# Optimization experiments

Measured on AMD Instinct MI355X. Metric: run time of the kernel, lower is better.

## Reference

```python
import jax, jax.numpy as jnp
import numpy as np

CHANNEL = 256
MEM_SIZE = 684
POS_NUM = 128
NEG_NUM = 512
TEMP = 1.0
CLASS_NUM = 60
BANK_ROWS = MEM_SIZE * CLASS_NUM  # 41040
BATCH = 512


def setup_inputs() -> dict:
    key = jax.random.key(0)
    k1, k2, k3, k4 = jax.random.split(key, 4)
    f = jax.random.normal(k1, (BATCH, CHANNEL), dtype=jnp.float32)
    f_normed = f / jnp.linalg.norm(f, axis=-1, keepdims=True)
    label = jax.random.randint(k2, (BATCH,), 0, CLASS_NUM, dtype=jnp.int32)
    bank = jax.random.normal(k3, (BANK_ROWS, CHANNEL), dtype=jnp.float32)
    bank = bank / jnp.linalg.norm(bank, axis=-1, keepdims=True)
    bank_flag = jnp.ones((BANK_ROWS,), dtype=jnp.float32)  # warmed-up bank
    rand_neg = jax.random.uniform(k4, (BATCH, BANK_ROWS), dtype=jnp.float32)
    # exact torch roundrobin enqueue logic (sequential over the batch)
    rr = np.zeros(CLASS_NUM, dtype=np.int64)
    idxs = []
    for i in np.asarray(label).tolist():
        rr[i] = rr[i] + 1 if rr[i] < CLASS_NUM - 1 else 0
        idxs.append(int(rr[i]) + i * MEM_SIZE)
    enqueue_idx = jnp.asarray(idxs, dtype=jnp.int32)
    return {"f_normed": f_normed, "label": label, "enqueue_idx": enqueue_idx,
            "bank": bank, "bank_flag": bank_flag, "rand_neg": rand_neg}


def reference(f_normed, label, enqueue_idx, bank, bank_flag, rand_neg):
    N = f_normed.shape[0]
    # enqueue (detached write, as in torch: Bank[indies] = f_normed.detach())
    bank = bank.at[enqueue_idx].set(jax.lax.stop_gradient(f_normed))
    flag = bank_flag.at[enqueue_idx].set(1.0)
    # all_pairs: [N, M]
    all_pairs = jnp.einsum('nc,mc->nm', f_normed, bank)
    bank_label = jnp.tile(jnp.arange(CLASS_NUM), MEM_SIZE)  # arange(C).repeat(mem)
    eq = label[:, None] == bank_label[None, :]
    valid = flag > 0
    pos_mask = eq & valid
    neg_mask = (~eq) & valid
    # hard positives: smallest POS_NUM positive similarities per row
    pos_hard = jnp.sort(jnp.where(pos_mask, all_pairs, jnp.inf), axis=-1)[:, :POS_NUM]
    # hard negatives: largest NEG_NUM negative similarities per row
    neg_hard, _ = jax.lax.top_k(jnp.where(neg_mask, all_pairs, -jnp.inf), NEG_NUM)
    # random negatives: uniform sample without replacement via noise argsort
    r = jnp.where(neg_mask, rand_neg, jnp.inf)
    rand_idx = jnp.argsort(r, axis=-1)[:, :NEG_NUM]
    neg_rand = jnp.take_along_axis(all_pairs, rand_idx, axis=-1)
    # combined logits: [N, 2*POS_NUM, 1+NEG_NUM]
    pos = pos_hard[:, :, None]
    h2h = jnp.concatenate([pos, jnp.broadcast_to(neg_hard[:, None, :], (N, POS_NUM, NEG_NUM))], axis=-1)
    h2r = jnp.concatenate([pos, jnp.broadcast_to(neg_rand[:, None, :], (N, POS_NUM, NEG_NUM))], axis=-1)
    combined = jnp.concatenate([h2h, h2r], axis=1).reshape(-1, 1 + NEG_NUM)
    # cross entropy with target class 0 for every row
    loss = -jnp.mean(jax.nn.log_softmax(combined / TEMP, axis=-1)[:, 0])
    return loss
```

## Files before the change

kernel.cpp:

```cpp
#include <hip/hip_runtime.h>

#define CH    256
#define MEM   684
#define POSN  128
#define NEGN  512
#define CLS   60
#define ROWS  41040
#define BATCHN 512

typedef unsigned int u32;
typedef unsigned short u16;
typedef unsigned long long u64;

typedef __attribute__((ext_vector_type(8))) short bf16x8;
typedef __attribute__((ext_vector_type(4))) float f32x4;

__device__ __forceinline__ float b2f(u16 u) { return __uint_as_float(((u32)u) << 16); }
__device__ __forceinline__ u16 f2b(float x) {
  u32 u = __float_as_uint(x);
  u32 r = ((u >> 16) & 1u) + 0x7FFFu;
  return (u16)((u + r) >> 16);
}
__device__ __forceinline__ u32 umin2(u32 a, u32 b) { return a < b ? a : b; }

#if defined(__has_builtin)
#if __has_builtin(__builtin_amdgcn_global_load_lds)
#define HAVE_GLL 1
#endif
#endif

__device__ __forceinline__ void stage16(const u16* g, u16* l) {
#ifdef HAVE_GLL
  __builtin_amdgcn_global_load_lds((const __attribute__((address_space(1))) void*)g,
                                   (__attribute__((address_space(3))) void*)l, 16, 0, 0);
#else
  *(uint4*)l = *(const uint4*)g;
#endif
}

__global__ __launch_bounds__(256) void k_convert(const float* __restrict__ bank,
                                                 u16* __restrict__ bankB) {
  size_t i = (size_t)(blockIdx.x * 256 + threadIdx.x) * 8;
  float4 a = *(const float4*)(bank + i);
  float4 b = *(const float4*)(bank + i + 4);
  uint4 o;
  o.x = (u32)f2b(a.x) | ((u32)f2b(a.y) << 16);
  o.y = (u32)f2b(a.z) | ((u32)f2b(a.w) << 16);
  o.z = (u32)f2b(b.x) | ((u32)f2b(b.y) << 16);
  o.w = (u32)f2b(b.z) | ((u32)f2b(b.w) << 16);
  *(uint4*)(bankB + i) = o;
}

__global__ __launch_bounds__(256) void k_scatter(const float* __restrict__ f,
                                                 const int* __restrict__ enq,
                                                 u16* __restrict__ fB,
                                                 u16* __restrict__ bankB) {
  int n = blockIdx.x, t = threadIdx.x;
  u16 v = f2b(f[n * CH + t]);
  fB[n * CH + t] = v;
  int row = enq[n];
  bankB[(size_t)row * CH + t] = v;
}

__global__ __launch_bounds__(256) void k_gemm(const u16* __restrict__ fB,
                                              const u16* __restrict__ bankB,
                                              u16* __restrict__ Cb) {
  __shared__ __align__(16) u16 As[128 * 32];
  __shared__ __align__(16) u16 Bs[128 * 32];
  const int tid = threadIdx.x;
  const int wave = tid >> 6, lane = tid & 63;

  const u32 id = blockIdx.x;
  const u32 q = 160u, r4 = 4u;
  const u32 xcd = id & 7u, jj = id >> 3;
  const u32 wg = (xcd < r4 ? xcd * (q + 1u) : r4 * (q + 1u) + (xcd - r4) * q) + jj;
  const int bm = (int)(wg & 3u) * 128;
  const int bn = (int)(wg >> 2) * 128;

  const int wm = (wave & 1) * 64, wn = (wave >> 1) * 64;
  const int m_in = lane & 15;
  const int ks = (lane >> 4) * 8;

  f32x4 acc[4][4] = {};

  for (int k0 = 0; k0 < CH; k0 += 32) {
    __syncthreads();
#pragma unroll
    for (int i = 0; i < 2; i++) {
      int u = tid + 256 * i;
      int row = u >> 2;
      int kk = (u & 3) * 8;
      stage16(fB + (size_t)(bm + row) * CH + k0 + kk, As + u * 8);
      int rb = bn + row;
      if (rb >= ROWS) rb = bn;
      stage16(bankB + (size_t)rb * CH + k0 + kk, Bs + u * 8);
    }
    __syncthreads();

    bf16x8 af[4], bf[4];
#pragma unroll
    for (int t4 = 0; t4 < 4; t4++) {
      af[t4] = *(const bf16x8*)(As + (wm + t4 * 16 + m_in) * 32 + ks);
      bf[t4] = *(const bf16x8*)(Bs + (wn + t4 * 16 + m_in) * 32 + ks);
    }
#pragma unroll
    for (int mi = 0; mi < 4; mi++)
#pragma unroll
      for (int ni = 0; ni < 4; ni++)
        acc[mi][ni] = __builtin_amdgcn_mfma_f32_16x16x32_bf16(bf[ni], af[mi], acc[mi][ni], 0, 0, 0);
  }

  const int cc = lane & 15;
  const int rr = (lane >> 4) * 4;
#pragma unroll
  for (int mi = 0; mi < 4; mi++) {
    const int row = bm + wm + mi * 16 + cc;
#pragma unroll
    for (int ni = 0; ni < 4; ni++) {
      const int n0 = bn + wn + ni * 16 + rr;
      if (n0 < ROWS) {
        u64 pk = (u64)f2b(acc[mi][ni][0]) | ((u64)f2b(acc[mi][ni][1]) << 16) |
                 ((u64)f2b(acc[mi][ni][2]) << 32) | ((u64)f2b(acc[mi][ni][3]) << 48);
        *(u64*)(Cb + (size_t)row * ROWS + n0) = pk;
      }
    }
  }
}

__device__ __forceinline__ u32 wscan_incl(u32 v) {
  int lane = (int)(threadIdx.x & 63);
#pragma unroll
  for (int off = 1; off < 64; off <<= 1) {
    u32 t = __shfl_up(v, off, 64);
    if (lane >= off) v += t;
  }
  return v;
}

__device__ __forceinline__ u32 scan1024(u32 v, u32* tmp, int tid) {
  u32 inc = wscan_incl(v);
  int wid = tid >> 6;
  if ((tid & 63) == 63) tmp[wid] = inc;
  __syncthreads();
  if (tid < 64) {
    u32 t = (tid < 16) ? tmp[tid] : 0u;
    u32 ti = wscan_incl(t);
    if (tid < 16) tmp[tid] = ti - t;
  }
  __syncthreads();
  u32 r = inc + tmp[wid];
  __syncthreads();
  return r;
}

__device__ __forceinline__ float redsum1024(float v, float* tmp, int tid) {
#pragma unroll
  for (int off = 32; off > 0; off >>= 1) v += __shfl_xor(v, off, 64);
  int wid = tid >> 6;
  if ((tid & 63) == 0) tmp[wid] = v;
  __syncthreads();
  if (tid == 0) {
    float t = 0.f;
#pragma unroll
    for (int i = 0; i < 16; i++) t += tmp[i];
    tmp[0] = t;
  }
  __syncthreads();
  float r = tmp[0];
  __syncthreads();
  return r;
}

__device__ __forceinline__ int binof(float v, float lo, float scale) {
  int b = (int)((v - lo) * scale);
  return b < 0 ? 0 : (b > 2047 ? 2047 : b);
}

#define VITER 5
#define VTAIL 80
#define VTAILBASE 40960
#define CAPC 3072
#define CAPR 1536

__global__ __launch_bounds__(1024, 8) void k_select(const u16* __restrict__ Cb,
                                                    const float* __restrict__ rnd,
                                                    const int* __restrict__ label,
                                                    float* __restrict__ partial) {
  const int n = blockIdx.x;
  const int tid = threadIdx.x;
  const u16* crow = Cb + (size_t)n * ROWS;
  const float* rrow = rnd + (size_t)n * ROWS;
  const int lab = label[n];

  __shared__ __align__(16) char smem[56448];
  u32* histc = (u32*)(smem);
  u32* histr = (u32*)(smem + 8192);
  float* clist = (float*)(smem + 16384);
  float* rl_rv = (float*)(smem + 28672);
  float* rl_cv = (float*)(smem + 34816);
  u32* rl_mi = (u32*)(smem + 40960);
  u32* stmp = (u32*)(smem + 47104);
  float* fred = (float*)(smem + 47104);
  float* cb_c = (float*)(smem + 51200);
  float* rb_r = (float*)(smem + 53248);
  float* rb_c = (float*)(smem + 54272);
  u32* rb_m = (u32*)(smem + 55296);
  u32* ctl = (u32*)(smem + 56320);
  float* bc_f = (float*)(ctl + 8);

  const int rv0 = (tid * 8) % 60;

  float T1 = 0.09375f;
  float T0 = 0.03125f;
  u32 F = 0, G = 0;
  float sc_c, sc_r;

  for (int attempt = 0;; attempt++) {
    for (int i = tid; i < 2048; i += 1024) { histc[i] = 0; histr[i] = 0; }
    if (tid == 0) { ctl[0] = 0; ctl[1] = 0; }
    __syncthreads();
    sc_c = 2048.0f / (1.0625f - T1);
    sc_r = 2048.0f / T0;
    int rb = rv0;
#pragma unroll 1
    for (int it = 0; it < VITER; it++) {
      int m8 = (it * 1024 + tid) * 8;
      uint4 cr = *(const uint4*)(crow + m8);
      float4 ra = *(const float4*)(rrow + m8);
      float4 rb4 = *(const float4*)(rrow + m8 + 4);
      u32 cw[4] = {cr.x, cr.y, cr.z, cr.w};
      float rs[8] = {ra.x, ra.y, ra.z, ra.w, rb4.x, rb4.y, rb4.z, rb4.w};
      u32 mc = 0, mr = 0;
      int r = rb;
#pragma unroll
      for (int j = 0; j < 8; j++) {
        bool isneg = (r != lab);
        float c = b2f((u16)(cw[j >> 1] >> ((j & 1) * 16)));
        if (isneg && c > T1) mc |= (1u << j);
        if (isneg && rs[j] < T0) mr |= (1u << j);
        r++;
        if (r == 60) r = 0;
      }
      u32 s1 = 0, s2 = 0;
      if (mc) s1 = atomicAdd(&ctl[0], (u32)__popc(mc));
      if (mr) s2 = atomicAdd(&ctl[1], (u32)__popc(mr));
#pragma unroll
      for (int j = 0; j < 8; j++) {
        if (mc & (1u << j)) {
          float c = b2f((u16)(cw[j >> 1] >> ((j & 1) * 16)));
          if (s1 < CAPC) clist[s1] = c;
          atomicAdd(&histc[binof(c, T1, sc_c)], 1u);
          s1++;
        }
        if (mr & (1u << j)) {
          float c = b2f((u16)(cw[j >> 1] >> ((j & 1) * 16)));
          if (s2 < CAPR) { rl_rv[s2] = rs[j]; rl_cv[s2] = c; rl_mi[s2] = (u32)(m8 + j); }
          atomicAdd(&histr[binof(rs[j], 0.0f, sc_r)], 1u);
          s2++;
        }
      }
      rb += 32;
      if (rb >= 60) rb -= 60;
    }
    if (tid < VTAIL) {
      int m = VTAILBASE + tid;
      int r = 40 + tid;
      if (r >= 60) r -= 60;
      bool isneg = (r != lab);
      float c = b2f(crow[m]);
      if (isneg && c > T1) {
        u32 s1 = atomicAdd(&ctl[0], 1u);
        if (s1 < CAPC) clist[s1] = c;
        atomicAdd(&histc[binof(c, T1, sc_c)], 1u);
      }
      float rv = rrow[m];
      if (isneg && rv < T0) {
        u32 s2 = atomicAdd(&ctl[1], 1u);
        if (s2 < CAPR) { rl_rv[s2] = rv; rl_cv[s2] = c; rl_mi[s2] = (u32)m; }
        atomicAdd(&histr[binof(rv, 0.0f, sc_r)], 1u);
      }
    }
    __syncthreads();
    F = ctl[0];
    G = ctl[1];
    __syncthreads();
    if (F >= NEGN && G >= NEGN) break;
    if (F < NEGN) T1 = -1.1f;
    if (G < NEGN) T0 = 1.1f;
  }
  const bool listc_ok = (F <= CAPC);
  const bool listr_ok = (G <= CAPR);

  if (tid == 0) { ctl[2] = 0; ctl[3] = 0; ctl[4] = 0; ctl[5] = 0; ctl[6] = 0; ctl[7] = 0; }
  u32 fsum = histc[tid * 2] + histc[tid * 2 + 1];
  u32 finc = scan1024(fsum, stmp, tid);
  u32 fexc = finc - fsum;
  u32 tcpos = F - NEGN + 1;
  if (fexc < tcpos && tcpos <= finc) {
    u32 run = fexc;
#pragma unroll
    for (int i = 0; i < 2; i++) {
      u32 h = histc[tid * 2 + i];
      if (run + h >= tcpos) { ctl[4] = (u32)(tid * 2 + i); ctl[5] = F - (run + h); break; }
      run += h;
    }
  }
  u32 gsum = histr[tid * 2] + histr[tid * 2 + 1];
  u32 ginc = scan1024(gsum, stmp, tid);
  u32 gexc = ginc - gsum;
  if (gexc < NEGN && NEGN <= ginc) {
    u32 run = gexc;
#pragma unroll
    for (int i = 0; i < 2; i++) {
      u32 h = histr[tid * 2 + i];
      if (run + h >= NEGN) { ctl[6] = (u32)(tid * 2 + i); ctl[7] = run; break; }
      run += h;
    }
  }
  __syncthreads();
  const u32 b_c = ctl[4], cnt_gt = ctl[5];
  const u32 b_r = ctl[6], cnt_lt = ctl[7];
  const u32 need_c = NEGN - cnt_gt;
  const u32 need_r = NEGN - cnt_lt;

  float sH = 0.f, sR = 0.f;
  if (listc_ok) {
    for (u32 i = tid; i < F; i += 1024) {
      float c = clist[i];
      u32 b = (u32)binof(c, T1, sc_c);
      if (b > b_c) sH += expf(c);
      else if (b == b_c) {
        u32 id = atomicAdd(&ctl[2], 1u);
        if (id < 512) cb_c[id] = c;
      }
    }
  }
  if (listr_ok) {
    for (u32 i = tid; i < G; i += 1024) {
      float rv = rl_rv[i];
      u32 b = (u32)binof(rv, 0.0f, sc_r);
      if (b < b_r) sR += expf(rl_cv[i]);
      else if (b == b_r) {
        u32 id = atomicAdd(&ctl[3], 1u);
        if (id < 256) { rb_r[id] = rv; rb_c[id] = rl_cv[i]; rb_m[id] = rl_mi[i]; }
      }
    }
  }
  if (!listc_ok || !listr_ok) {
    for (int m = tid; m < ROWS; m += 1024) {
      int r = m % 60;
      if (r == lab) continue;
      float c = b2f(crow[m]);
      if (!listc_ok && c > T1) {
        u32 b = (u32)binof(c, T1, sc_c);
        if (b > b_c) sH += expf(c);
        else if (b == b_c) {
          u32 id = atomicAdd(&ctl[2], 1u);
          if (id < 512) cb_c[id] = c;
        }
      }
      if (!listr_ok) {
        float rv = rrow[m];
        if (rv < T0) {
          u32 b = (u32)binof(rv, 0.0f, sc_r);
          if (b < b_r) sR += expf(c);
          else if (b == b_r) {
            u32 id = atomicAdd(&ctl[3], 1u);
            if (id < 256) { rb_r[id] = rv; rb_c[id] = c; rb_m[id] = (u32)m; }
          }
        }
      }
    }
  }
  __syncthreads();
  float SHsum = redsum1024(sH, fred, tid);
  float SRsum = redsum1024(sR, fred, tid);

  if (tid == 0) {
    float addH = 0.f;
    u32 Lc = umin2(ctl[2], 512u);
    u32 kc = umin2(need_c, Lc);
    for (u32 k = 0; k < kc; k++) {
      int best = 0;
      float bv = -3.0e38f;
      for (u32 i = 0; i < Lc; i++)
        if (cb_c[i] > bv) { bv = cb_c[i]; best = (int)i; }
      cb_c[best] = -3.0e38f;
      addH += expf(bv);
    }
    u32 Lr = umin2(ctl[3], 256u);
    for (u32 i = 1; i < Lr; i++) {
      float rv = rb_r[i]; u32 mm = rb_m[i]; float cv = rb_c[i];
      int j = (int)i - 1;
      while (j >= 0 && (rb_r[j] > rv || (rb_r[j] == rv && rb_m[j] > mm))) {
        rb_r[j + 1] = rb_r[j]; rb_m[j + 1] = rb_m[j]; rb_c[j + 1] = rb_c[j];
        j--;
      }
      rb_r[j + 1] = rv; rb_m[j + 1] = mm; rb_c[j + 1] = cv;
    }
    float addR = 0.f;
    u32 kr = umin2(need_r, Lr);
    for (u32 i = 0; i < kr; i++) addR += expf(rb_c[i]);
    bc_f[0] = addH;
    bc_f[1] = addR;
  }
  __syncthreads();
  const float S_H = SHsum + bc_f[0];
  const float S_R = SRsum + bc_f[1];
  __syncthreads();

  float pval = 0.f;
  int pbin = 0;
  const bool hasp = tid < MEM;
  const float PLO = -1.03125f;
  const float PSC = 2048.0f / 2.09375f;
  if (hasp) {
    pval = b2f(crow[lab + CLS * tid]);
    pbin = binof(pval, PLO, PSC);
  }
  for (int i = tid; i < 2048; i += 1024) histc[i] = 0;
  if (tid == 0) { ctl[2] = 0; ctl[4] = 0; ctl[5] = 0; }
  __syncthreads();
  if (hasp) atomicAdd(&histc[pbin], 1u);
  __syncthreads();
  u32 hsum = histc[tid * 2] + histc[tid * 2 + 1];
  u32 hinc = scan1024(hsum, stmp, tid);
  u32 hexc = hinc - hsum;
  if (hexc < POSN && POSN <= hinc) {
    u32 run = hexc;
#pragma unroll
    for (int i = 0; i < 2; i++) {
      u32 h = histc[tid * 2 + i];
      if (run + h >= POSN) { ctl[4] = (u32)(tid * 2 + i); ctl[5] = run; break; }
      run += h;
    }
  }
  __syncthreads();
  const u32 b_p = ctl[4], cnt_below = ctl[5];
  const u32 need_p = POSN - cnt_below;
  if (hasp && (u32)pbin == b_p) {
    u32 id = atomicAdd(&ctl[2], 1u);
    if (id < 512) cb_c[id] = pval;
  }
  float term = 0.f;
  if (hasp && (u32)pbin < b_p) {
    float e = expf(pval);
    term = (pval - logf(e + S_H)) + (pval - logf(e + S_R));
  }
  __syncthreads();
  if (tid == 0) {
// ... 13 lines not shown
  }
  __syncthreads();
  float tot = redsum1024(term, fred, tid);
  if (tid == 0) partial[n] = tot + bc_f[0];
}

__global__ __launch_bounds__(256) void k_final(const float* __restrict__ partial,
                                               float* __restrict__ out) {
  __shared__ float fred[256];
  int tid = threadIdx.x;
  float v = partial[tid] + partial[tid + 256];
  fred[tid] = v;
  __syncthreads();
  for (int off = 128; off > 0; off >>= 1) {
    if (tid < off) fred[tid] += fred[tid + off];
    __syncthreads();
  }
  if (tid == 0) out[0] = -fred[0] / (float)(BATCHN * 2 * POSN);
}

extern "C" void kernel_launch(void* const* d_in, const int* in_sizes, int n_in,
                              void* d_out, int out_size, void* d_ws, size_t ws_size,
                              hipStream_t stream) {
  const float* f = (const float*)d_in[0];
  const int* label = (const int*)d_in[1];
  const int* enq = (const int*)d_in[2];
  const float* bank = (const float*)d_in[3];
  const float* rnd = (const float*)d_in[5];
  float* out = (float*)d_out;

  char* ws = (char*)d_ws;
  u16* bankB = (u16*)ws;
  u16* fB = (u16*)(ws + 21012480);
  u16* Cb = (u16*)(ws + 21012480 + 262144);
  float* partial = (float*)(ws + 21012480 + 262144 + 42024960);

  k_convert<<<dim3(5130), dim3(256), 0, stream>>>(bank, bankB);
  k_scatter<<<dim3(BATCHN), dim3(256), 0, stream>>>(f, enq, fB, bankB);
  k_gemm<<<dim3(1284), dim3(256), 0, stream>>>(fB, bankB, Cb);
  k_select<<<dim3(BATCHN), dim3(1024), 0, stream>>>(Cb, rnd, label, partial);
  k_final<<<dim3(1), dim3(256), 0, stream>>>(partial, out);
}
```

Measured before the change: 236.4 us.

## Fuse candidate filtering into GEMM epilogue and compact lists in global memory

The GEMM epilogue now reads the random-noise values, applies the fixed thresholds, and appends hard-negative candidates, random-negative candidates and positive similarities into per-row compacted global lists using atomic counters. The select kernel then builds its histograms from these short lists instead of rescanning the full 41040-element similarity and noise rows, and falls back to the old full scan only when a count is out of range. This trades a second full pass over the similarity and noise matrices for extra reads of the noise matrix, scattered atomics and scattered stores in the GEMM epilogue, plus a memset before launch. List order is now nondeterministic, which may matter only for tie handling.

```diff
diff --git a/kernel.cpp b/kernel.cpp
--- a/kernel.cpp
+++ b/kernel.cpp
@@ -22,6 +22,11 @@
   return (u16)((u + r) >> 16);
 }
 __device__ __forceinline__ u32 umin2(u32 a, u32 b) { return a < b ? a : b; }
+
+#define T1BASE 0.09375f
+#define T0BASE 0.03125f
+#define CAPC 3072
+#define CAPR 1536
 
 #if defined(__has_builtin)
 #if __has_builtin(__builtin_amdgcn_global_load_lds)
@@ -64,7 +69,16 @@
 
 __global__ __launch_bounds__(256) void k_gemm(const u16* __restrict__ fB,
                                               const u16* __restrict__ bankB,
-                                              u16* __restrict__ Cb) {
+                                              const float* __restrict__ rnd,
+                                              const int* __restrict__ label,
+                                              u16* __restrict__ Cb,
+                                              u32* __restrict__ cnt_c,
+                                              u32* __restrict__ cnt_r,
+                                              u16* __restrict__ clist_g,
+                                              float* __restrict__ rrv_g,
+                                              u16* __restrict__ rcv_g,
+                                              u32* __restrict__ rmi_g,
+                                              u16* __restrict__ pos_g) {
   __shared__ __align__(16) u16 As[128 * 32];
   __shared__ __align__(16) u16 Bs[128 * 32];
   const int tid = threadIdx.x;
@@ -115,13 +129,53 @@
 #pragma unroll
   for (int mi = 0; mi < 4; mi++) {
     const int row = bm + wm + mi * 16 + cc;
+    const int labr = label[row];
 #pragma unroll
     for (int ni = 0; ni < 4; ni++) {
       const int n0 = bn + wn + ni * 16 + rr;
       if (n0 < ROWS) {
-        u64 pk = (u64)f2b(acc[mi][ni][0]) | ((u64)f2b(acc[mi][ni][1]) << 16) |
-                 ((u64)f2b(acc[mi][ni][2]) << 32) | ((u64)f2b(acc[mi][ni][3]) << 48);
+        u16 h0 = f2b(acc[mi][ni][0]), h1 = f2b(acc[mi][ni][1]);
+        u16 h2 = f2b(acc[mi][ni][2]), h3 = f2b(acc[mi][ni][3]);
+        u64 pk = (u64)h0 | ((u64)h1 << 16) | ((u64)h2 << 32) | ((u64)h3 << 48);
         *(u64*)(Cb + (size_t)row * ROWS + n0) = pk;
+
+        float4 rv4 = *(const float4*)(rnd + (size_t)row * ROWS + n0);
+        u16 hs[4] = {h0, h1, h2, h3};
+        float rs[4] = {rv4.x, rv4.y, rv4.z, rv4.w};
+        u32 mcc = 0, mrr = 0;
+        int r = n0 % 60;
+#pragma unroll
+        for (int qq = 0; qq < 4; qq++) {
+          bool neg = (r != labr);
+          float cv = b2f(hs[qq]);
+          if (neg && cv > T1BASE) mcc |= (1u << qq);
+          if (neg && rs[qq] < T0BASE) mrr |= (1u << qq);
+          if (r == labr) pos_g[row * MEM + (n0 + qq) / 60] = hs[qq];
+          r++;
+          if (r == 60) r = 0;
+        }
+        if (mcc) {
+          u32 base = atomicAdd(&cnt_c[row], (u32)__popc(mcc));
+#pragma unroll
+          for (int qq = 0; qq < 4; qq++)
+            if (mcc & (1u << qq)) {
+              if (base < CAPC) clist_g[(size_t)row * CAPC + base] = hs[qq];
+              base++;
+            }
+        }
+        if (mrr) {
+          u32 base = atomicAdd(&cnt_r[row], (u32)__popc(mrr));
+#pragma unroll
+          for (int qq = 0; qq < 4; qq++)
+            if (mrr & (1u << qq)) {
+              if (base < CAPR) {
+                rrv_g[(size_t)row * CAPR + base] = rs[qq];
+                rcv_g[(size_t)row * CAPR + base] = hs[qq];
+                rmi_g[(size_t)row * CAPR + base] = (u32)(n0 + qq);
+              }
+              base++;
+            }
+        }
       }
     }
   }
@@ -179,12 +233,17 @@
 #define VITER 5
 #define VTAIL 80
 #define VTAILBASE 40960
-#define CAPC 3072
-#define CAPR 1536
 
 __global__ __launch_bounds__(1024, 8) void k_select(const u16* __restrict__ Cb,
                                                     const float* __restrict__ rnd,
                                                     const int* __restrict__ label,
+                                                    const u32* __restrict__ cnt_c,
+                                                    const u32* __restrict__ cnt_r,
+                                                    const u16* __restrict__ clist_g,
+                                                    const float* __restrict__ rrv_g,
+                                                    const u16* __restrict__ rcv_g,
+                                                    const u32* __restrict__ rmi_g,
+                                                    const u16* __restrict__ pos_g,
                                                     float* __restrict__ partial) {
   const int n = blockIdx.x;
   const int tid = threadIdx.x;
@@ -208,88 +267,101 @@
   u32* ctl = (u32*)(smem + 56320);
   float* bc_f = (float*)(ctl + 8);
 
-  const int rv0 = (tid * 8) % 60;
-
-  float T1 = 0.09375f;
-  float T0 = 0.03125f;
-  u32 F = 0, G = 0;
-  float sc_c, sc_r;
-
-  for (int attempt = 0;; attempt++) {
+  float T1 = T1BASE;
+  float T0 = T0BASE;
+  u32 F = cnt_c[n];
+  u32 G = cnt_r[n];
+  float sc_c = 2048.0f / (1.0625f - T1);
+  float sc_r = 2048.0f / T0;
+  bool listc_ok = true, listr_ok = true;
+  const bool fast = (F >= NEGN && G >= NEGN && F <= CAPC && G <= CAPR);
+
+  if (fast) {
     for (int i = tid; i < 2048; i += 1024) { histc[i] = 0; histr[i] = 0; }
-    if (tid == 0) { ctl[0] = 0; ctl[1] = 0; }
     __syncthreads();
-    sc_c = 2048.0f / (1.0625f - T1);
-    sc_r = 2048.0f / T0;
-    int rb = rv0;
+    for (u32 i = tid; i < F; i += 1024)
+      atomicAdd(&histc[binof(b2f(clist_g[(size_t)n * CAPC + i]), T1, sc_c)], 1u);
+    for (u32 i = tid; i < G; i += 1024)
+      atomicAdd(&histr[binof(rrv_g[(size_t)n * CAPR + i], 0.0f, sc_r)], 1u);
+    __syncthreads();
+  } else {
+    const int rv0 = (tid * 8) % 60;
+    for (int attempt = 0;; attempt++) {
+      for (int i = tid; i < 2048; i += 1024) { histc[i] = 0; histr[i] = 0; }
+      if (tid == 0) { ctl[0] = 0; ctl[1] = 0; }
+      __syncthreads();
+      sc_c = 2048.0f / (1.0625f - T1);
+      sc_r = 2048.0f / T0;
+      int rb = rv0;
 #pragma unroll 1
-    for (int it = 0; it < VITER; it++) {
-      int m8 = (it * 1024 + tid) * 8;
-      uint4 cr = *(const uint4*)(crow + m8);
-      float4 ra = *(const float4*)(rrow + m8);
-      float4 rb4 = *(const float4*)(rrow + m8 + 4);
-      u32 cw[4] = {cr.x, cr.y, cr.z, cr.w};
-      float rs[8] = {ra.x, ra.y, ra.z, ra.w, rb4.x, rb4.y, rb4.z, rb4.w};
-      u32 mc = 0, mr = 0;
-      int r = rb;
-#pragma unroll
-      for (int j = 0; j < 8; j++) {
+      for (int it = 0; it < VITER; it++) {
+        int m8 = (it * 1024 + tid) * 8;
+        uint4 cr = *(const uint4*)(crow + m8);
+        float4 ra = *(const float4*)(rrow + m8);
+        float4 rb4 = *(const float4*)(rrow + m8 + 4);
+        u32 cw[4] = {cr.x, cr.y, cr.z, cr.w};
+        float rs[8] = {ra.x, ra.y, ra.z, ra.w, rb4.x, rb4.y, rb4.z, rb4.w};
+        u32 mc = 0, mr = 0;
+        int r = rb;
+#pragma unroll
+        for (int j = 0; j < 8; j++) {
+          bool isneg = (r != lab);
+          float c = b2f((u16)(cw[j >> 1] >> ((j & 1) * 16)));
+          if (isneg && c > T1) mc |= (1u << j);
+          if (isneg && rs[j] < T0) mr |= (1u << j);
+          r++;
+          if (r == 60) r = 0;
+        }
+        u32 s1 = 0, s2 = 0;
+        if (mc) s1 = atomicAdd(&ctl[0], (u32)__popc(mc));
+        if (mr) s2 = atomicAdd(&ctl[1], (u32)__popc(mr));
+#pragma unroll
+        for (int j = 0; j < 8; j++) {
+          if (mc & (1u << j)) {
+            float c = b2f((u16)(cw[j >> 1] >> ((j & 1) * 16)));
+            if (s1 < CAPC) clist[s1] = c;
+            atomicAdd(&histc[binof(c, T1, sc_c)], 1u);
+            s1++;
+          }
+          if (mr & (1u << j)) {
+            float c = b2f((u16)(cw[j >> 1] >> ((j & 1) * 16)));
+            if (s2 < CAPR) { rl_rv[s2] = rs[j]; rl_cv[s2] = c; rl_mi[s2] = (u32)(m8 + j); }
+            atomicAdd(&histr[binof(rs[j], 0.0f, sc_r)], 1u);
+            s2++;
+          }
+        }
+        rb += 32;
+        if (rb >= 60) rb -= 60;
+      }
+      if (tid < VTAIL) {
+        int m = VTAILBASE + tid;
+        int r = 40 + tid;
+        if (r >= 60) r -= 60;
         bool isneg = (r != lab);
-        float c = b2f((u16)(cw[j >> 1] >> ((j & 1) * 16)));
-        if (isneg && c > T1) mc |= (1u << j);
-        if (isneg && rs[j] < T0) mr |= (1u << j);
-        r++;
-        if (r == 60) r = 0;
-      }
-      u32 s1 = 0, s2 = 0;
-      if (mc) s1 = atomicAdd(&ctl[0], (u32)__popc(mc));
-      if (mr) s2 = atomicAdd(&ctl[1], (u32)__popc(mr));
-#pragma unroll
-      for (int j = 0; j < 8; j++) {
-        if (mc & (1u << j)) {
-          float c = b2f((u16)(cw[j >> 1] >> ((j & 1) * 16)));
+        float c = b2f(crow[m]);
+        if (isneg && c > T1) {
+          u32 s1 = atomicAdd(&ctl[0], 1u);
           if (s1 < CAPC) clist[s1] = c;
           atomicAdd(&histc[binof(c, T1, sc_c)], 1u);
-          s1++;
-        }
-        if (mr & (1u << j)) {
-          float c = b2f((u16)(cw[j >> 1] >> ((j & 1) * 16)));
-          if (s2 < CAPR) { rl_rv[s2] = rs[j]; rl_cv[s2] = c; rl_mi[s2] = (u32)(m8 + j); }
-          atomicAdd(&histr[binof(rs[j], 0.0f, sc_r)], 1u);
-          s2++;
-        }
-      }
-      rb += 32;
-      if (rb >= 60) rb -= 60;
-    }
-    if (tid < VTAIL) {
-      int m = VTAILBASE + tid;
-      int r = 40 + tid;
-      if (r >= 60) r -= 60;
-      bool isneg = (r != lab);
-      float c = b2f(crow[m]);
-      if (isneg && c > T1) {
-        u32 s1 = atomicAdd(&ctl[0], 1u);
-        if (s1 < CAPC) clist[s1] = c;
-        atomicAdd(&histc[binof(c, T1, sc_c)], 1u);
-      }
-      float rv = rrow[m];
-      if (isneg && rv < T0) {
-        u32 s2 = atomicAdd(&ctl[1], 1u);
-        if (s2 < CAPR) { rl_rv[s2] = rv; rl_cv[s2] = c; rl_mi[s2] = (u32)m; }
-        atomicAdd(&histr[binof(rv, 0.0f, sc_r)], 1u);
-      }
-    }
-    __syncthreads();
-    F = ctl[0];
-    G = ctl[1];
-    __syncthreads();
-    if (F >= NEGN && G >= NEGN) break;
-    if (F < NEGN) T1 = -1.1f;
-    if (G < NEGN) T0 = 1.1f;
-  }
-  const bool listc_ok = (F <= CAPC);
-  const bool listr_ok = (G <= CAPR);
+        }
+        float rv = rrow[m];
+        if (isneg && rv < T0) {
+          u32 s2 = atomicAdd(&ctl[1], 1u);
+          if (s2 < CAPR) { rl_rv[s2] = rv; rl_cv[s2] = c; rl_mi[s2] = (u32)m; }
+          atomicAdd(&histr[binof(rv, 0.0f, sc_r)], 1u);
+        }
+      }
+      __syncthreads();
+      F = ctl[0];
+      G = ctl[1];
+      __syncthreads();
+      if (F >= NEGN && G >= NEGN) break;
+      if (F < NEGN) T1 = -1.1f;
+      if (G < NEGN) T0 = 1.1f;
+    }
+    listc_ok = (F <= CAPC);
+    listr_ok = (G <= CAPR);
+  }
 
   if (tid == 0) { ctl[2] = 0; ctl[3] = 0; ctl[4] = 0; ctl[5] = 0; ctl[6] = 0; ctl[7] = 0; }
   u32 fsum = histc[tid * 2] + histc[tid * 2 + 1];
@@ -324,9 +396,9 @@
   const u32 need_r = NEGN - cnt_lt;
 
   float sH = 0.f, sR = 0.f;
-  if (listc_ok) {
+  if (fast) {
     for (u32 i = tid; i < F; i += 1024) {
-      float c = clist[i];
+      float c = b2f(clist_g[(size_t)n * CAPC + i]);
       u32 b = (u32)binof(c, T1, sc_c);
       if (b > b_c) sH += expf(c);
       else if (b == b_c) {
@@ -334,24 +406,23 @@
         if (id < 512) cb_c[id] = c;
       }
     }
-  }
-  if (listr_ok) {
     for (u32 i = tid; i < G; i += 1024) {
-      float rv = rl_rv[i];
+      float rv = rrv_g[(size_t)n * CAPR + i];
       u32 b = (u32)binof(rv, 0.0f, sc_r);
-      if (b < b_r) sR += expf(rl_cv[i]);
+      if (b < b_r) sR += expf(b2f(rcv_g[(size_t)n * CAPR + i]));
       else if (b == b_r) {
         u32 id = atomicAdd(&ctl[3], 1u);
-        if (id < 256) { rb_r[id] = rv; rb_c[id] = rl_cv[i]; rb_m[id] = rl_mi[i]; }
-      }
-    }
-  }
-  if (!listc_ok || !listr_ok) {
-    for (int m = tid; m < ROWS; m += 1024) {
-      int r = m % 60;
-      if (r == lab) continue;
-      float c = b2f(crow[m]);
-      if (!listc_ok && c > T1) {
+        if (id < 256) {
+          rb_r[id] = rv;
+          rb_c[id] = b2f(rcv_g[(size_t)n * CAPR + i]);
+          rb_m[id] = rmi_g[(size_t)n * CAPR + i];
+        }
+      }
+    }
+  } else {
+    if (listc_ok) {
+      for (u32 i = tid; i < F; i += 1024) {
+        float c = clist[i];
         u32 b = (u32)binof(c, T1, sc_c);
         if (b > b_c) sH += expf(c);
         else if (b == b_c) {
@@ -359,14 +430,40 @@
           if (id < 512) cb_c[id] = c;
         }
       }
-      if (!listr_ok) {
-        float rv = rrow[m];
-        if (rv < T0) {
-          u32 b = (u32)binof(rv, 0.0f, sc_r);
-          if (b < b_r) sR += expf(c);
-          else if (b == b_r) {
-            u32 id = atomicAdd(&ctl[3], 1u);
-            if (id < 256) { rb_r[id] = rv; rb_c[id] = c; rb_m[id] = (u32)m; }
+    }
+    if (listr_ok) {
+      for (u32 i = tid; i < G; i += 1024) {
+        float rv = rl_rv[i];
+        u32 b = (u32)binof(rv, 0.0f, sc_r);
+        if (b < b_r) sR += expf(rl_cv[i]);
+        else if (b == b_r) {
+          u32 id = atomicAdd(&ctl[3], 1u);
+          if (id < 256) { rb_r[id] = rv; rb_c[id] = rl_cv[i]; rb_m[id] = rl_mi[i]; }
+        }
+      }
+    }
+    if (!listc_ok || !listr_ok) {
+      for (int m = tid; m < ROWS; m += 1024) {
+        int r = m % 60;
+        if (r == lab) continue;
+        float c = b2f(crow[m]);
+        if (!listc_ok && c > T1) {
+          u32 b = (u32)binof(c, T1, sc_c);
+          if (b > b_c) sH += expf(c);
+          else if (b == b_c) {
+            u32 id = atomicAdd(&ctl[2], 1u);
+            if (id < 512) cb_c[id] = c;
+          }
+        }
+        if (!listr_ok) {
+          float rv = rrow[m];
+          if (rv < T0) {
+            u32 b = (u32)binof(rv, 0.0f, sc_r);
+            if (b < b_r) sR += expf(c);
+            else if (b == b_r) {
+              u32 id = atomicAdd(&ctl[3], 1u);
+              if (id < 256) { rb_r[id] = rv; rb_c[id] = c; rb_m[id] = (u32)m; }
+            }
           }
         }
       }
@@ -415,7 +512,7 @@
   const float PLO = -1.03125f;
   const float PSC = 2048.0f / 2.09375f;
   if (hasp) {
-    pval = b2f(crow[lab + CLS * tid]);
+    pval = b2f(pos_g[n * MEM + tid]);
     pbin = binof(pval, PLO, PSC);
   }
   for (int i = tid; i < 2048; i += 1024) histc[i] = 0;
@@ -495,12 +592,25 @@
   char* ws = (char*)d_ws;
   u16* bankB = (u16*)ws;
   u16* fB = (u16*)(ws + 21012480);
-  u16* Cb = (u16*)(ws + 21012480 + 262144);
-  float* partial = (float*)(ws + 21012480 + 262144 + 42024960);
+  u16* Cb = (u16*)(ws + 21274624);
+  float* partial = (float*)(ws + 63299584);
+  u32* cnt_c = (u32*)(ws + 63301632);
+  u32* cnt_r = (u32*)(ws + 63303680);
+  u16* clist_g = (u16*)(ws + 63305728);
+  float* rrv_g = (float*)(ws + 66451456);
+  u16* rcv_g = (u16*)(ws + 69597184);
+  u32* rmi_g = (u32*)(ws + 71170048);
+  u16* pos_g = (u16*)(ws + 74315776);
+
+  hipMemsetAsync(cnt_c, 0, 4096, stream);
 
   k_convert<<<dim3(5130), dim3(256), 0, stream>>>(bank, bankB);
   k_scatter<<<dim3(BATCHN), dim3(256), 0, stream>>>(f, enq, fB, bankB);
-  k_gemm<<<dim3(1284), dim3(256), 0, stream>>>(fB, bankB, Cb);
-  k_select<<<dim3(BATCHN), dim3(1024), 0, stream>>>(Cb, rnd, label, partial);
+  k_gemm<<<dim3(1284), dim3(256), 0, stream>>>(fB, bankB, rnd, label, Cb,
+                                               cnt_c, cnt_r, clist_g, rrv_g,
+                                               rcv_g, rmi_g, pos_g);
+  k_select<<<dim3(BATCHN), dim3(1024), 0, stream>>>(Cb, rnd, label, cnt_c, cnt_r,
+                                                    clist_g, rrv_g, rcv_g, rmi_g,
+                                                    pos_g, partial);
   k_final<<<dim3(1), dim3(256), 0, stream>>>(partial, out);
 }
```

New measurement: 602.1 us. +154.7%, slower.

## Fuse hard-negative histogram and random-negative candidate capture into GEMM epilogue

Applied to the files above, without the earlier changes.

The GEMM epilogue now builds a per-row global histogram of high-similarity bf16 values (exact bf16 bins above a threshold), collects random-negative candidates whose noise is below a threshold into per-row global lists, and writes the positive similarities into a compact array. The select kernel uses these precomputed structures on a fast path instead of rescanning the full 41040-wide row of similarities and noise, and falls back to the old scan on overflow. This removes a full re-read of the similarity and random matrices in the select stage. In exchange the GEMM epilogue does many global atomics, reads the random matrix, does per-element integer divides, and needs an extra memset, which could slow the GEMM.

```diff
diff --git a/kernel.cpp b/kernel.cpp
--- a/kernel.cpp
+++ b/kernel.cpp
@@ -22,6 +22,14 @@
   return (u16)((u + r) >> 16);
 }
 __device__ __forceinline__ u32 umin2(u32 a, u32 b) { return a < b ? a : b; }
+
+#define T1BASE 0.09375f
+#define T0BASE 0.03125f
+#define NBINC 512
+#define BASEC 0x3DC1u
+#define CAPC 3072
+#define CAPR 1536
+#define LCAP 16
 
 #if defined(__has_builtin)
 #if __has_builtin(__builtin_amdgcn_global_load_lds)
@@ -64,9 +72,24 @@
 
 __global__ __launch_bounds__(256) void k_gemm(const u16* __restrict__ fB,
                                               const u16* __restrict__ bankB,
-                                              u16* __restrict__ Cb) {
-  __shared__ __align__(16) u16 As[128 * 32];
-  __shared__ __align__(16) u16 Bs[128 * 32];
+                                              const float* __restrict__ rnd,
+                                              const int* __restrict__ label,
+                                              u16* __restrict__ Cb,
+                                              u32* __restrict__ histc_g,
+                                              u32* __restrict__ cnt_r,
+                                              u32* __restrict__ ovf,
+                                              float* __restrict__ rrv_g,
+                                              u16* __restrict__ rcv_g,
+                                              u16* __restrict__ rmi_g,
+                                              u16* __restrict__ pos_g) {
+  __shared__ __align__(16) char lds_pool[16896];
+  u16* As = (u16*)lds_pool;
+  u16* Bs = As + 128 * 32;
+  u32* lcnt = (u32*)lds_pool;
+  float* lrv = (float*)(lds_pool + 512);
+  u16* lcv = (u16*)(lds_pool + 8704);
+  u16* lmi = (u16*)(lds_pool + 12800);
+
   const int tid = threadIdx.x;
   const int wave = tid >> 6, lane = tid & 63;
 
@@ -110,18 +133,72 @@
         acc[mi][ni] = __builtin_amdgcn_mfma_f32_16x16x32_bf16(bf[ni], af[mi], acc[mi][ni], 0, 0, 0);
   }
 
+  __syncthreads();
+  if (tid < 128) lcnt[tid] = 0;
+  __syncthreads();
+
   const int cc = lane & 15;
   const int rr = (lane >> 4) * 4;
 #pragma unroll
   for (int mi = 0; mi < 4; mi++) {
     const int row = bm + wm + mi * 16 + cc;
+    const int rlocal = wm + mi * 16 + cc;
+    const int labr = label[row];
 #pragma unroll
     for (int ni = 0; ni < 4; ni++) {
       const int n0 = bn + wn + ni * 16 + rr;
       if (n0 < ROWS) {
-        u64 pk = (u64)f2b(acc[mi][ni][0]) | ((u64)f2b(acc[mi][ni][1]) << 16) |
-                 ((u64)f2b(acc[mi][ni][2]) << 32) | ((u64)f2b(acc[mi][ni][3]) << 48);
+        u16 h0 = f2b(acc[mi][ni][0]), h1 = f2b(acc[mi][ni][1]);
+        u16 h2 = f2b(acc[mi][ni][2]), h3 = f2b(acc[mi][ni][3]);
+        u64 pk = (u64)h0 | ((u64)h1 << 16) | ((u64)h2 << 32) | ((u64)h3 << 48);
         *(u64*)(Cb + (size_t)row * ROWS + n0) = pk;
+
+        float4 rv4 = *(const float4*)(rnd + (size_t)row * ROWS + n0);
+        u16 hs[4] = {h0, h1, h2, h3};
+        float rs[4] = {rv4.x, rv4.y, rv4.z, rv4.w};
+#pragma unroll
+        for (int qq = 0; qq < 4; qq++) {
+          int col = n0 + qq;
+          int j60 = col / 60;
+          int rmod = col - j60 * 60;
+          u16 hb = hs[qq];
+          if (rmod == labr) {
+            pos_g[row * MEM + j60] = hb;
+          } else {
+            if (hb > 0x3DC0u && hb < 0x8000u) {
+              u32 bin = (u32)hb - BASEC;
+              if (bin < NBINC) atomicAdd(&histc_g[((u32)row << 9) + bin], 1u);
+              else ovf[row] = 1;
+            }
+            if (rs[qq] < T0BASE) {
+              u32 s = atomicAdd(&lcnt[rlocal], 1u);
+              if (s < LCAP) {
+                lrv[rlocal * LCAP + s] = rs[qq];
+                lcv[rlocal * LCAP + s] = hb;
+                lmi[rlocal * LCAP + s] = (u16)col;
+              }
+            }
+          }
+        }
+      }
+    }
+  }
+  __syncthreads();
+  if (tid < 128) {
+    u32 cnt = lcnt[tid];
+    if (cnt) {
+      int grow = bm + tid;
+      u32 stored = umin2(cnt, (u32)LCAP);
+      if (cnt > LCAP) ovf[grow] = 1;
+      u32 base = atomicAdd(&cnt_r[grow], stored);
+      if (base + stored <= CAPR) {
+        for (u32 i = 0; i < stored; i++) {
+          rrv_g[(size_t)grow * CAPR + base + i] = lrv[tid * LCAP + i];
+          rcv_g[(size_t)grow * CAPR + base + i] = lcv[tid * LCAP + i];
+          rmi_g[(size_t)grow * CAPR + base + i] = lmi[tid * LCAP + i];
+        }
+      } else {
+        ovf[grow] = 1;
       }
     }
   }
@@ -179,12 +256,17 @@
 #define VITER 5
 #define VTAIL 80
 #define VTAILBASE 40960
-#define CAPC 3072
-#define CAPR 1536
 
 __global__ __launch_bounds__(1024, 8) void k_select(const u16* __restrict__ Cb,
                                                     const float* __restrict__ rnd,
                                                     const int* __restrict__ label,
+                                                    const u32* __restrict__ histc_g,
+                                                    const u32* __restrict__ cnt_r,
+                                                    const u32* __restrict__ ovf,
+                                                    const float* __restrict__ rrv_g,
+                                                    const u16* __restrict__ rcv_g,
+                                                    const u16* __restrict__ rmi_g,
+                                                    const u16* __restrict__ pos_g,
                                                     float* __restrict__ partial) {
   const int n = blockIdx.x;
   const int tid = threadIdx.x;
@@ -208,150 +290,209 @@
   u32* ctl = (u32*)(smem + 56320);
   float* bc_f = (float*)(ctl + 8);
 
-  const int rv0 = (tid * 8) % 60;
-
-  float T1 = 0.09375f;
-  float T0 = 0.03125f;
-  u32 F = 0, G = 0;
-  float sc_c, sc_r;
-
-  for (int attempt = 0;; attempt++) {
-    for (int i = tid; i < 2048; i += 1024) { histc[i] = 0; histr[i] = 0; }
-    if (tid == 0) { ctl[0] = 0; ctl[1] = 0; }
-    __syncthreads();
-    sc_c = 2048.0f / (1.0625f - T1);
-    sc_r = 2048.0f / T0;
-    int rb = rv0;
+  const u32 G0 = cnt_r[n];
+  const u32 ov = ovf[n];
+
+  const u32* hrow = histc_g + ((u32)n << 9);
+  u32 cbc = (tid < NBINC) ? hrow[tid] : 0u;
+  u32 cinc = scan1024(cbc, stmp, tid);
+  u32 cexc = cinc - cbc;
+  if (tid == 1023) ctl[0] = cinc;
+  __syncthreads();
+  const u32 Fh = ctl[0];
+  const bool fast = (ov == 0u) && Fh >= NEGN && G0 >= NEGN && G0 <= CAPR;
+
+  float S_H, S_R;
+  if (fast) {
+    if (tid == 0) { ctl[3] = 0; ctl[4] = 0; ctl[5] = 0; ctl[6] = 0; ctl[7] = 0; }
+    __syncthreads();
+    u32 tcpos = Fh - NEGN + 1;
+    if (tid < NBINC && cexc < tcpos && tcpos <= cinc) {
+      ctl[4] = (u32)tid;
+      ctl[5] = Fh - cinc;
+    }
+    __syncthreads();
+    const u32 b_c = ctl[4], cnt_gt = ctl[5];
+    const u32 need_c = NEGN - cnt_gt;
+    float sH = 0.f;
+    if (tid < NBINC && (u32)tid > b_c && cbc)
+      sH = (float)cbc * expf(b2f((u16)(BASEC + (u32)tid)));
+    float SHsum = redsum1024(sH, fred, tid);
+    S_H = SHsum + (float)need_c * expf(b2f((u16)(BASEC + b_c)));
+
+    for (int i = tid; i < 2048; i += 1024) histr[i] = 0;
+    __syncthreads();
+    const float sc_r = 2048.0f / T0BASE;
+    for (u32 i = tid; i < G0; i += 1024)
+      atomicAdd(&histr[binof(rrv_g[(size_t)n * CAPR + i], 0.0f, sc_r)], 1u);
+    __syncthreads();
+    u32 gsum = histr[tid * 2] + histr[tid * 2 + 1];
+    u32 ginc = scan1024(gsum, stmp, tid);
+    u32 gexc = ginc - gsum;
+    if (gexc < NEGN && NEGN <= ginc) {
+      u32 run = gexc;
+#pragma unroll
+      for (int i = 0; i < 2; i++) {
+        u32 h = histr[tid * 2 + i];
+        if (run + h >= NEGN) { ctl[6] = (u32)(tid * 2 + i); ctl[7] = run; break; }
+        run += h;
+      }
+    }
+    __syncthreads();
+    const u32 b_r = ctl[6], cnt_lt = ctl[7];
+    const u32 need_r = NEGN - cnt_lt;
+    float sR = 0.f;
+    for (u32 i = tid; i < G0; i += 1024) {
+      float rv = rrv_g[(size_t)n * CAPR + i];
+      u32 b = (u32)binof(rv, 0.0f, sc_r);
+      if (b < b_r) sR += expf(b2f(rcv_g[(size_t)n * CAPR + i]));
+      else if (b == b_r) {
+        u32 id = atomicAdd(&ctl[3], 1u);
+        if (id < 256) {
+          rb_r[id] = rv;
+          rb_c[id] = b2f(rcv_g[(size_t)n * CAPR + i]);
+          rb_m[id] = (u32)rmi_g[(size_t)n * CAPR + i];
+        }
+      }
+    }
+    __syncthreads();
+    float SRsum = redsum1024(sR, fred, tid);
+    if (tid == 0) {
+      u32 Lr = umin2(ctl[3], 256u);
+      for (u32 i = 1; i < Lr; i++) {
+        float rv = rb_r[i]; u32 mm = rb_m[i]; float cv = rb_c[i];
+        int j = (int)i - 1;
+        while (j >= 0 && (rb_r[j] > rv || (rb_r[j] == rv && rb_m[j] > mm))) {
+          rb_r[j + 1] = rb_r[j]; rb_m[j + 1] = rb_m[j]; rb_c[j + 1] = rb_c[j];
+          j--;
+        }
+        rb_r[j + 1] = rv; rb_m[j + 1] = mm; rb_c[j + 1] = cv;
+      }
+      float addR = 0.f;
+      u32 kr = umin2(need_r, Lr);
+      for (u32 i = 0; i < kr; i++) addR += expf(rb_c[i]);
+      bc_f[1] = addR;
+    }
+    __syncthreads();
+    S_R = SRsum + bc_f[1];
+    __syncthreads();
+  } else {
+    float T1 = T1BASE, T0 = T0BASE;
+    u32 F = 0, G = 0;
+    float sc_c, sc_r;
+    const int rv0 = (tid * 8) % 60;
+    for (int attempt = 0;; attempt++) {
+      for (int i = tid; i < 2048; i += 1024) { histc[i] = 0; histr[i] = 0; }
+      if (tid == 0) { ctl[0] = 0; ctl[1] = 0; }
+      __syncthreads();
+      sc_c = 2048.0f / (1.0625f - T1);
+      sc_r = 2048.0f / T0;
+      int rb = rv0;
 #pragma unroll 1
-    for (int it = 0; it < VITER; it++) {
-      int m8 = (it * 1024 + tid) * 8;
-      uint4 cr = *(const uint4*)(crow + m8);
-      float4 ra = *(const float4*)(rrow + m8);
-      float4 rb4 = *(const float4*)(rrow + m8 + 4);
-      u32 cw[4] = {cr.x, cr.y, cr.z, cr.w};
-      float rs[8] = {ra.x, ra.y, ra.z, ra.w, rb4.x, rb4.y, rb4.z, rb4.w};
-      u32 mc = 0, mr = 0;
-      int r = rb;
-#pragma unroll
-      for (int j = 0; j < 8; j++) {
+      for (int it = 0; it < VITER; it++) {
+        int m8 = (it * 1024 + tid) * 8;
+        uint4 cr = *(const uint4*)(crow + m8);
+        float4 ra = *(const float4*)(rrow + m8);
+        float4 rb4 = *(const float4*)(rrow + m8 + 4);
+        u32 cw[4] = {cr.x, cr.y, cr.z, cr.w};
+        float rs[8] = {ra.x, ra.y, ra.z, ra.w, rb4.x, rb4.y, rb4.z, rb4.w};
+        u32 mc = 0, mr = 0;
+        int r = rb;
+#pragma unroll
+        for (int j = 0; j < 8; j++) {
+          bool isneg = (r != lab);
+          float c = b2f((u16)(cw[j >> 1] >> ((j & 1) * 16)));
+          if (isneg && c > T1) mc |= (1u << j);
+          if (isneg && rs[j] < T0) mr |= (1u << j);
+          r++;
+          if (r == 60) r = 0;
+        }
+        u32 s1 = 0, s2 = 0;
+        if (mc) s1 = atomicAdd(&ctl[0], (u32)__popc(mc));
+        if (mr) s2 = atomicAdd(&ctl[1], (u32)__popc(mr));
+#pragma unroll
+        for (int j = 0; j < 8; j++) {
+          if (mc & (1u << j)) {
+            float c = b2f((u16)(cw[j >> 1] >> ((j & 1) * 16)));
+            if (s1 < CAPC) clist[s1] = c;
+            atomicAdd(&histc[binof(c, T1, sc_c)], 1u);
+            s1++;
+          }
+          if (mr & (1u << j)) {
+            float c = b2f((u16)(cw[j >> 1] >> ((j & 1) * 16)));
+            if (s2 < CAPR) { rl_rv[s2] = rs[j]; rl_cv[s2] = c; rl_mi[s2] = (u32)(m8 + j); }
+            atomicAdd(&histr[binof(rs[j], 0.0f, sc_r)], 1u);
+            s2++;
+          }
+        }
+        rb += 32;
+        if (rb >= 60) rb -= 60;
+      }
+      if (tid < VTAIL) {
+        int m = VTAILBASE + tid;
+        int r = 40 + tid;
+        if (r >= 60) r -= 60;
         bool isneg = (r != lab);
-        float c = b2f((u16)(cw[j >> 1] >> ((j & 1) * 16)));
-        if (isneg && c > T1) mc |= (1u << j);
-        if (isneg && rs[j] < T0) mr |= (1u << j);
-        r++;
-        if (r == 60) r = 0;
-      }
-      u32 s1 = 0, s2 = 0;
-      if (mc) s1 = atomicAdd(&ctl[0], (u32)__popc(mc));
-      if (mr) s2 = atomicAdd(&ctl[1], (u32)__popc(mr));
-#pragma unroll
-      for (int j = 0; j < 8; j++) {
-        if (mc & (1u << j)) {
-          float c = b2f((u16)(cw[j >> 1] >> ((j & 1) * 16)));
+        float c = b2f(crow[m]);
+        if (isneg && c > T1) {
+          u32 s1 = atomicAdd(&ctl[0], 1u);
           if (s1 < CAPC) clist[s1] = c;
           atomicAdd(&histc[binof(c, T1, sc_c)], 1u);
-          s1++;
-        }
-        if (mr & (1u << j)) {
-          float c = b2f((u16)(cw[j >> 1] >> ((j & 1) * 16)));
-          if (s2 < CAPR) { rl_rv[s2] = rs[j]; rl_cv[s2] = c; rl_mi[s2] = (u32)(m8 + j); }
-          atomicAdd(&histr[binof(rs[j], 0.0f, sc_r)], 1u);
-          s2++;
-        }
-      }
-      rb += 32;
-      if (rb >= 60) rb -= 60;
-    }
-    if (tid < VTAIL) {
-      int m = VTAILBASE + tid;
-      int r = 40 + tid;
-      if (r >= 60) r -= 60;
-      bool isneg = (r != lab);
-      float c = b2f(crow[m]);
-      if (isneg && c > T1) {
-        u32 s1 = atomicAdd(&ctl[0], 1u);
-        if (s1 < CAPC) clist[s1] = c;
-        atomicAdd(&histc[binof(c, T1, sc_c)], 1u);
-      }
-      float rv = rrow[m];
-      if (isneg && rv < T0) {
-        u32 s2 = atomicAdd(&ctl[1], 1u);
-        if (s2 < CAPR) { rl_rv[s2] = rv; rl_cv[s2] = c; rl_mi[s2] = (u32)m; }
-        atomicAdd(&histr[binof(rv, 0.0f, sc_r)], 1u);
-      }
-    }
-    __syncthreads();
-    F = ctl[0];
-    G = ctl[1];
-    __syncthreads();
-    if (F >= NEGN && G >= NEGN) break;
-    if (F < NEGN) T1 = -1.1f;
-    if (G < NEGN) T0 = 1.1f;
-  }
-  const bool listc_ok = (F <= CAPC);
-  const bool listr_ok = (G <= CAPR);
-
-  if (tid == 0) { ctl[2] = 0; ctl[3] = 0; ctl[4] = 0; ctl[5] = 0; ctl[6] = 0; ctl[7] = 0; }
-  u32 fsum = histc[tid * 2] + histc[tid * 2 + 1];
-  u32 finc = scan1024(fsum, stmp, tid);
-  u32 fexc = finc - fsum;
-  u32 tcpos = F - NEGN + 1;
-  if (fexc < tcpos && tcpos <= finc) {
-    u32 run = fexc;
-#pragma unroll
-    for (int i = 0; i < 2; i++) {
-      u32 h = histc[tid * 2 + i];
-      if (run + h >= tcpos) { ctl[4] = (u32)(tid * 2 + i); ctl[5] = F - (run + h); break; }
-      run += h;
-    }
-  }
-  u32 gsum = histr[tid * 2] + histr[tid * 2 + 1];
-  u32 ginc = scan1024(gsum, stmp, tid);
-  u32 gexc = ginc - gsum;
-  if (gexc < NEGN && NEGN <= ginc) {
-    u32 run = gexc;
-#pragma unroll
-    for (int i = 0; i < 2; i++) {
-      u32 h = histr[tid * 2 + i];
-      if (run + h >= NEGN) { ctl[6] = (u32)(tid * 2 + i); ctl[7] = run; break; }
-      run += h;
-    }
-  }
-  __syncthreads();
-  const u32 b_c = ctl[4], cnt_gt = ctl[5];
-  const u32 b_r = ctl[6], cnt_lt = ctl[7];
-  const u32 need_c = NEGN - cnt_gt;
-  const u32 need_r = NEGN - cnt_lt;
-
-  float sH = 0.f, sR = 0.f;
-  if (listc_ok) {
-    for (u32 i = tid; i < F; i += 1024) {
-      float c = clist[i];
-      u32 b = (u32)binof(c, T1, sc_c);
-      if (b > b_c) sH += expf(c);
-      else if (b == b_c) {
-        u32 id = atomicAdd(&ctl[2], 1u);
-        if (id < 512) cb_c[id] = c;
-      }
-    }
-  }
-  if (listr_ok) {
-    for (u32 i = tid; i < G; i += 1024) {
-      float rv = rl_rv[i];
-      u32 b = (u32)binof(rv, 0.0f, sc_r);
-      if (b < b_r) sR += expf(rl_cv[i]);
-      else if (b == b_r) {
-        u32 id = atomicAdd(&ctl[3], 1u);
-        if (id < 256) { rb_r[id] = rv; rb_c[id] = rl_cv[i]; rb_m[id] = rl_mi[i]; }
-      }
-    }
-  }
-  if (!listc_ok || !listr_ok) {
-    for (int m = tid; m < ROWS; m += 1024) {
-      int r = m % 60;
-      if (r == lab) continue;
-      float c = b2f(crow[m]);
-      if (!listc_ok && c > T1) {
+        }
+        float rv = rrow[m];
+        if (isneg && rv < T0) {
+          u32 s2 = atomicAdd(&ctl[1], 1u);
+          if (s2 < CAPR) { rl_rv[s2] = rv; rl_cv[s2] = c; rl_mi[s2] = (u32)m; }
+          atomicAdd(&histr[binof(rv, 0.0f, sc_r)], 1u);
+        }
+      }
+      __syncthreads();
+      F = ctl[0];
+      G = ctl[1];
+      __syncthreads();
+      if (F >= NEGN && G >= NEGN) break;
+      if (F < NEGN) T1 = -1.1f;
+      if (G < NEGN) T0 = 1.1f;
+    }
+    const bool listc_ok = (F <= CAPC);
+    const bool listr_ok = (G <= CAPR);
+
+    if (tid == 0) { ctl[2] = 0; ctl[3] = 0; ctl[4] = 0; ctl[5] = 0; ctl[6] = 0; ctl[7] = 0; }
+    u32 fsum = histc[tid * 2] + histc[tid * 2 + 1];
+    u32 finc = scan1024(fsum, stmp, tid);
+    u32 fexc = finc - fsum;
+    u32 tcpos = F - NEGN + 1;
+    if (fexc < tcpos && tcpos <= finc) {
+      u32 run = fexc;
+#pragma unroll
+      for (int i = 0; i < 2; i++) {
+        u32 h = histc[tid * 2 + i];
+        if (run + h >= tcpos) { ctl[4] = (u32)(tid * 2 + i); ctl[5] = F - (run + h); break; }
+        run += h;
+      }
+    }
+    u32 gsum = histr[tid * 2] + histr[tid * 2 + 1];
+    u32 ginc = scan1024(gsum, stmp, tid);
+    u32 gexc = ginc - gsum;
+    if (gexc < NEGN && NEGN <= ginc) {
+      u32 run = gexc;
+#pragma unroll
+      for (int i = 0; i < 2; i++) {
+        u32 h = histr[tid * 2 + i];
+        if (run + h >= NEGN) { ctl[6] = (u32)(tid * 2 + i); ctl[7] = run; break; }
+        run += h;
+      }
+    }
+    __syncthreads();
+    const u32 b_c = ctl[4], cnt_gt = ctl[5];
+    const u32 b_r = ctl[6], cnt_lt = ctl[7];
+    const u32 need_c = NEGN - cnt_gt;
+    const u32 need_r = NEGN - cnt_lt;
+
+    float sH = 0.f, sR = 0.f;
+    if (listc_ok) {
+      for (u32 i = tid; i < F; i += 1024) {
+        float c = clist[i];
         u32 b = (u32)binof(c, T1, sc_c);
         if (b > b_c) sH += expf(c);
         else if (b == b_c) {
@@ -359,55 +500,81 @@
           if (id < 512) cb_c[id] = c;
         }
       }
-      if (!listr_ok) {
-        float rv = rrow[m];
-        if (rv < T0) {
-          u32 b = (u32)binof(rv, 0.0f, sc_r);
-          if (b < b_r) sR += expf(c);
-          else if (b == b_r) {
-            u32 id = atomicAdd(&ctl[3], 1u);
-            if (id < 256) { rb_r[id] = rv; rb_c[id] = c; rb_m[id] = (u32)m; }
+    }
+    if (listr_ok) {
+      for (u32 i = tid; i < G; i += 1024) {
+        float rv = rl_rv[i];
+        u32 b = (u32)binof(rv, 0.0f, sc_r);
+        if (b < b_r) sR += expf(rl_cv[i]);
+        else if (b == b_r) {
+          u32 id = atomicAdd(&ctl[3], 1u);
+          if (id < 256) { rb_r[id] = rv; rb_c[id] = rl_cv[i]; rb_m[id] = rl_mi[i]; }
+        }
+      }
+    }
+    if (!listc_ok || !listr_ok) {
+      for (int m = tid; m < ROWS; m += 1024) {
+        int r = m % 60;
+        if (r == lab) continue;
+        float c = b2f(crow[m]);
+        if (!listc_ok && c > T1) {
+          u32 b = (u32)binof(c, T1, sc_c);
+          if (b > b_c) sH += expf(c);
+          else if (b == b_c) {
+            u32 id = atomicAdd(&ctl[2], 1u);
+            if (id < 512) cb_c[id] = c;
           }
         }
-      }
-    }
-  }
-  __syncthreads();
-  float SHsum = redsum1024(sH, fred, tid);
-  float SRsum = redsum1024(sR, fred, tid);
-
-  if (tid == 0) {
-    float addH = 0.f;
-    u32 Lc = umin2(ctl[2], 512u);
-    u32 kc = umin2(need_c, Lc);
-    for (u32 k = 0; k < kc; k++) {
-      int best = 0;
-      float bv = -3.0e38f;
-      for (u32 i = 0; i < Lc; i++)
-        if (cb_c[i] > bv) { bv = cb_c[i]; best = (int)i; }
-      cb_c[best] = -3.0e38f;
-      addH += expf(bv);
-    }
-    u32 Lr = umin2(ctl[3], 256u);
-    for (u32 i = 1; i < Lr; i++) {
-      float rv = rb_r[i]; u32 mm = rb_m[i]; float cv = rb_c[i];
-      int j = (int)i - 1;
-      while (j >= 0 && (rb_r[j] > rv || (rb_r[j] == rv && rb_m[j] > mm))) {
-        rb_r[j + 1] = rb_r[j]; rb_m[j + 1] = rb_m[j]; rb_c[j + 1] = rb_c[j];
-        j--;
-      }
-      rb_r[j + 1] = rv; rb_m[j + 1] = mm; rb_c[j + 1] = cv;
-    }
-    float addR = 0.f;
-    u32 kr = umin2(need_r, Lr);
-    for (u32 i = 0; i < kr; i++) addR += expf(rb_c[i]);
-    bc_f[0] = addH;
-    bc_f[1] = addR;
-  }
-  __syncthreads();
-  const float S_H = SHsum + bc_f[0];
-  const float S_R = SRsum + bc_f[1];
-  __syncthreads();
+        if (!listr_ok) {
+          float rv = rrow[m];
+          if (rv < T0) {
+            u32 b = (u32)binof(rv, 0.0f, sc_r);
+            if (b < b_r) sR += expf(c);
+            else if (b == b_r) {
+              u32 id = atomicAdd(&ctl[3], 1u);
+              if (id < 256) { rb_r[id] = rv; rb_c[id] = c; rb_m[id] = (u32)m; }
+            }
+          }
+        }
+      }
+    }
+    __syncthreads();
+    float SHsum = redsum1024(sH, fred, tid);
+    float SRsum = redsum1024(sR, fred, tid);
+
+    if (tid == 0) {
+      float addH = 0.f;
+      u32 Lc = umin2(ctl[2], 512u);
+      u32 kc = umin2(need_c, Lc);
+      for (u32 k = 0; k < kc; k++) {
+        int best = 0;
+        float bv = -3.0e38f;
+        for (u32 i = 0; i < Lc; i++)
+          if (cb_c[i] > bv) { bv = cb_c[i]; best = (int)i; }
+        cb_c[best] = -3.0e38f;
+        addH += expf(bv);
+      }
+      u32 Lr = umin2(ctl[3], 256u);
+      for (u32 i = 1; i < Lr; i++) {
+        float rv = rb_r[i]; u32 mm = rb_m[i]; float cv = rb_c[i];
+        int j = (int)i - 1;
+        while (j >= 0 && (rb_r[j] > rv || (rb_r[j] == rv && rb_m[j] > mm))) {
+          rb_r[j + 1] = rb_r[j]; rb_m[j + 1] = rb_m[j]; rb_c[j + 1] = rb_c[j];
+          j--;
+        }
+        rb_r[j + 1] = rv; rb_m[j + 1] = mm; rb_c[j + 1] = cv;
+      }
+      float addR = 0.f;
+      u32 kr = umin2(need_r, Lr);
+      for (u32 i = 0; i < kr; i++) addR += expf(rb_c[i]);
+      bc_f[0] = addH;
+      bc_f[1] = addR;
+    }
+    __syncthreads();
+    S_H = SHsum + bc_f[0];
+    S_R = SRsum + bc_f[1];
+    __syncthreads();
+  }
 
   float pval = 0.f;
   int pbin = 0;
@@ -415,7 +582,7 @@
   const float PLO = -1.03125f;
   const float PSC = 2048.0f / 2.09375f;
   if (hasp) {
-    pval = b2f(crow[lab + CLS * tid]);
+    pval = b2f(pos_g[n * MEM + tid]);
     pbin = binof(pval, PLO, PSC);
   }
   for (int i = tid; i < 2048; i += 1024) histc[i] = 0;
@@ -495,12 +662,25 @@
   char* ws = (char*)d_ws;
   u16* bankB = (u16*)ws;
   u16* fB = (u16*)(ws + 21012480);
-  u16* Cb = (u16*)(ws + 21012480 + 262144);
-  float* partial = (float*)(ws + 21012480 + 262144 + 42024960);
+  u16* Cb = (u16*)(ws + 21274624);
+  float* partial = (float*)(ws + 63299584);
+  u32* histc_g = (u32*)(ws + 63301632);
+  u32* cnt_r = (u32*)(ws + 64350208);
+  u32* ovf = (u32*)(ws + 64352256);
+  float* rrv_g = (float*)(ws + 64354304);
+  u16* rcv_g = (u16*)(ws + 67500032);
+  u16* rmi_g = (u16*)(ws + 69072896);
+  u16* pos_g = (u16*)(ws + 70645760);
+
+  hipMemsetAsync(histc_g, 0, 1052672, stream);
 
   k_convert<<<dim3(5130), dim3(256), 0, stream>>>(bank, bankB);
   k_scatter<<<dim3(BATCHN), dim3(256), 0, stream>>>(f, enq, fB, bankB);
-  k_gemm<<<dim3(1284), dim3(256), 0, stream>>>(fB, bankB, Cb);
-  k_select<<<dim3(BATCHN), dim3(1024), 0, stream>>>(Cb, rnd, label, partial);
+  k_gemm<<<dim3(1284), dim3(256), 0, stream>>>(fB, bankB, rnd, label, Cb,
+                                               histc_g, cnt_r, ovf, rrv_g,
+                                               rcv_g, rmi_g, pos_g);
+  k_select<<<dim3(BATCHN), dim3(1024), 0, stream>>>(Cb, rnd, label, histc_g, cnt_r,
+                                                    ovf, rrv_g, rcv_g, rmi_g,
+                                                    pos_g, partial);
   k_final<<<dim3(1), dim3(256), 0, stream>>>(partial, out);
 }
```

Result: slower. 289.3 us (+22.4%).
